# Optimization experiments

Measured on AMD Instinct MI355X. Metric: run time of the kernel, lower is better.

## Reference

```python
import jax, jax.numpy as jnp
import numpy as np

B, T1, T2 = 4, 768, 256
T = T1 + T2            # n_token
NI = T2                # n_i_token
D = 1024               # n_embd
H_MLP = 4096           # n_mlp_hidden
L = 12                 # n_layer
V = 512                # num_class / vocab_size
EPS = 1e-5


def _ln(x, g, b):
    m = jnp.mean(x, axis=-1, keepdims=True)
    v = jnp.mean((x - m) ** 2, axis=-1, keepdims=True)
    return (x - m) * jax.lax.rsqrt(v + EPS) * g + b


def setup_inputs() -> dict:
    key = jax.random.key(0)
    ks = jax.random.split(key, 16)
    s = 0.02
    return {
        "xt": jax.random.randint(ks[0], (B, T1), 0, V, dtype=jnp.int32),
        "zi": jax.random.randint(ks[1], (B, T2), 0, V, dtype=jnp.int32),
        "pos_emb": jax.random.normal(ks[2], (T, D), jnp.float32) * s,
        "t_emb": jax.random.normal(ks[3], (V, D), jnp.float32) * s,
        "i_emb": jax.random.normal(ks[4], (V, D), jnp.float32) * s,
        "ln1_g": jnp.ones((L, D), jnp.float32),
        "ln1_b": jnp.zeros((L, D), jnp.float32),
        "Wq": jax.random.normal(ks[5], (L, D, D), jnp.float32) * s,
        "Wk": jax.random.normal(ks[6], (L, D, D), jnp.float32) * s,
        "Wv": jax.random.normal(ks[7], (L, D, D), jnp.float32) * s,
        "ln2_g": jnp.ones((L, D), jnp.float32),
        "ln2_b": jnp.zeros((L, D), jnp.float32),
        "W1": jax.random.normal(ks[8], (L, D, H_MLP), jnp.float32) * s,
        "b1": jnp.zeros((L, H_MLP), jnp.float32),
        "W2": jax.random.normal(ks[9], (L, H_MLP, D), jnp.float32) * s,
        "b2": jnp.zeros((L, D), jnp.float32),
        "ro_W": jax.random.normal(ks[10], (D, V), jnp.float32) * s,
        "ro_b": jnp.zeros((V,), jnp.float32),
    }


def reference(xt, zi, pos_emb, t_emb, i_emb, ln1_g, ln1_b, Wq, Wk, Wv,
              ln2_g, ln2_b, W1, b1, W2, b2, ro_W, ro_b):
    # token + position embeddings: [B, T, D]
    H0 = jnp.concatenate([i_emb[zi], t_emb[xt]], axis=1) + pos_emb[None]
    scale = 1.0 / np.sqrt(D).astype(np.float32)

    def layer(H, p):
        g1, b1_, wq, wk, wv, g2, b2_, w1, bb1, w2, bb2 = p
        H1 = _ln(H, g1, b1_)
        q = H1 @ wq  # [B, T, D]
        k = H1 @ wk
        v = H1 @ wv
        attn = jax.nn.softmax(jnp.einsum('bid,bjd->bij', q, k) * scale, axis=-1)
        H = H + jnp.einsum('bij,bjd->bid', attn, v)
        # second application with extra rescale by embedding dim (H.shape[2] == D)
        H = H + jnp.einsum('bij,bjd->bid', attn / D, v)
        H2 = _ln(H, g2, b2_)
        H = H + jax.nn.gelu(H2 @ w1 + bb1, approximate=False) @ w2 + bb2
        return H, None

    params = (ln1_g, ln1_b, Wq, Wk, Wv, ln2_g, ln2_b, W1, b1, W2, b2)
    H, _ = jax.lax.scan(layer, H0, params)
    prediction = H @ ro_W + ro_b  # [B, T, V]
    return prediction[:, NI:, :]
```

## Files before the change

### kernel.cpp

```cpp
#include <hip/hip_runtime.h>
#include <hip/hip_bf16.h>
#include <math.h>

#define D_EMB  1024
#define T_TOK  1024
#define T1_TOK 768
#define T2_TOK 256
#define HMLP   4096
#define NLAYER 12
#define VCLS   512

typedef __attribute__((ext_vector_type(8))) short          short8;
typedef __attribute__((ext_vector_type(4))) float          f32x4;
typedef __attribute__((ext_vector_type(4))) unsigned short us4;
typedef unsigned short us;

__device__ __forceinline__ us f2bf(float f) {
    union { float f; unsigned int u; } c; c.f = f;
    unsigned int u = c.u;
    return (us)((u + 0x7FFFu + ((u >> 16) & 1u)) >> 16);
}

__device__ __forceinline__ void gld_lds16(const us* g, us* l) {
    __builtin_amdgcn_global_load_lds(
        (__attribute__((address_space(1))) void*)g,
        (__attribute__((address_space(3))) void*)l, 16, 0, 0);
}

__global__ __launch_bounds__(256)
void embed_kernel(const int* __restrict__ xt, const int* __restrict__ zi,
                  const float* __restrict__ pos, const float* __restrict__ temb,
                  const float* __restrict__ iemb, float* __restrict__ H)
{
    const long idx = (long)blockIdx.x * 256 + threadIdx.x;
    const long e   = idx * 4;
    const int  dd  = (int)(e & (D_EMB - 1));
    const long bt  = e >> 10;
    const int  t   = (int)(bt & (T_TOK - 1));
    const int  b   = (int)(bt >> 10);
    const float* src;
    if (t < T2_TOK) src = iemb + (long)zi[b * T2_TOK + t] * D_EMB + dd;
    else            src = temb + (long)xt[b * T1_TOK + (t - T2_TOK)] * D_EMB + dd;
    float4 sv = *(const float4*)src;
    float4 pv = *(const float4*)(pos + (long)t * D_EMB + dd);
    float4 o; o.x = sv.x + pv.x; o.y = sv.y + pv.y; o.z = sv.z + pv.z; o.w = sv.w + pv.w;
    *(float4*)(H + e) = o;
}

__global__ __launch_bounds__(256)
void ln_kernel(const float* __restrict__ X, const float* __restrict__ g,
               const float* __restrict__ b, us* __restrict__ Y)
{
    const long row = blockIdx.x;
    const int  tid = threadIdx.x;
    float4 v = *(const float4*)(X + row * D_EMB + tid * 4);
    float s = v.x + v.y + v.z + v.w;
    float q = v.x*v.x + v.y*v.y + v.z*v.z + v.w*v.w;
    #pragma unroll
    for (int o = 32; o >= 1; o >>= 1) { s += __shfl_down(s, o); q += __shfl_down(q, o); }
    __shared__ float rs[4], rq[4];
    const int w = tid >> 6;
    if ((tid & 63) == 0) { rs[w] = s; rq[w] = q; }
    __syncthreads();
    s = rs[0] + rs[1] + rs[2] + rs[3];
    q = rq[0] + rq[1] + rq[2] + rq[3];
    const float mean = s * (1.0f / D_EMB);
    const float var  = q * (1.0f / D_EMB) - mean * mean;
    const float rstd = rsqrtf(var + 1e-5f);
    float4 gg = *(const float4*)(g + tid * 4);
    float4 bb = *(const float4*)(b + tid * 4);
    us4 o;
    o.x = f2bf((v.x - mean) * rstd * gg.x + bb.x);
    o.y = f2bf((v.y - mean) * rstd * gg.y + bb.y);
    o.z = f2bf((v.z - mean) * rstd * gg.z + bb.z);
    o.w = f2bf((v.w - mean) * rstd * gg.w + bb.w);
    *(us4*)(Y + row * D_EMB + tid * 4) = o;
}

__global__ __launch_bounds__(256)
void softmax_kernel(const float* __restrict__ S, us* __restrict__ P)
{
    const long row = blockIdx.x;
    const int  tid = threadIdx.x;
    float4 v = *(const float4*)(S + row * T_TOK + tid * 4);
    const float sc = 0.03125f;
    float a = v.x * sc, b = v.y * sc, c = v.z * sc, d = v.w * sc;
    float mx = fmaxf(fmaxf(a, b), fmaxf(c, d));
    #pragma unroll
    for (int o = 32; o >= 1; o >>= 1) mx = fmaxf(mx, __shfl_down(mx, o));
    __shared__ float rm[4], rsum[4];
    const int w = tid >> 6;
    if ((tid & 63) == 0) rm[w] = mx;
    __syncthreads();
    mx = fmaxf(fmaxf(rm[0], rm[1]), fmaxf(rm[2], rm[3]));
    float e0 = expf(a - mx), e1 = expf(b - mx), e2 = expf(c - mx), e3 = expf(d - mx);
    float s = e0 + e1 + e2 + e3;
    #pragma unroll
    for (int o = 32; o >= 1; o >>= 1) s += __shfl_down(s, o);
    if ((tid & 63) == 0) rsum[w] = s;
    __syncthreads();
    s = rsum[0] + rsum[1] + rsum[2] + rsum[3];
    const float inv = 1.0f / s;
    us4 o4; o4.x = f2bf(e0 * inv); o4.y = f2bf(e1 * inv);
    o4.z = f2bf(e2 * inv); o4.w = f2bf(e3 * inv);
    *(us4*)(P + row * T_TOK + tid * 4) = o4;
}

__global__ __launch_bounds__(256)
void convT_kernel(const float* __restrict__ src, us* __restrict__ dst,
                  int K, int N)
{
    __shared__ us tile[32][33];
    const int tn = blockIdx.x, tk = blockIdx.y;
    const int tx = threadIdx.x & 31, ty = threadIdx.x >> 5;
    #pragma unroll
    for (int i = 0; i < 4; ++i) {
        const int r = ty + i * 8;
        tile[r][tx] = f2bf(src[(long)(tk * 32 + r) * N + tn * 32 + tx]);
    }
    __syncthreads();
    #pragma unroll
    for (int i = 0; i < 4; ++i) {
        const int r = ty + i * 8;
        dst[(long)(tn * 32 + r) * K + tk * 32 + tx] = tile[tx][r];
    }
}

__global__ __launch_bounds__(256)
void wconv_kernel(const float* __restrict__ Wq, const float* __restrict__ Wk,
                  const float* __restrict__ Wv, const float* __restrict__ W1,
                  const float* __restrict__ W2,
                  us* __restrict__ WqT, us* __restrict__ WkT,
                  us* __restrict__ WvT, us* __restrict__ W1T,
                  us* __restrict__ W2T)
{
    __shared__ us tile[64][66];
    const int t = blockIdx.x;
    const float* src; us* dst; int K, N, tk, tn;
    if (t < 768) {
        const int wsel = t >> 8, tt = t & 255;
        src = (wsel == 0) ? Wq : (wsel == 1) ? Wk : Wv;
        dst = (wsel == 0) ? WqT : (wsel == 1) ? WkT : WvT;
        K = 1024; N = 1024; tk = tt >> 4; tn = tt & 15;
    } else if (t < 1792) {
        const int tt = t - 768;
        src = W1; dst = W1T; K = 1024; N = 4096; tk = tt >> 6; tn = tt & 63;
    } else {
        const int tt = t - 1792;
        src = W2; dst = W2T; K = 4096; N = 1024; tk = tt >> 4; tn = tt & 15;
    }
    const int r  = threadIdx.x >> 4;
    const int c4 = threadIdx.x & 15;
    #pragma unroll
    for (int i = 0; i < 4; ++i) {
        const int row = r + i * 16;
        float4 v = *(const float4*)(src + (long)(tk * 64 + row) * N + tn * 64 + c4 * 4);
        tile[row][c4 * 4 + 0] = f2bf(v.x);
        tile[row][c4 * 4 + 1] = f2bf(v.y);
        tile[row][c4 * 4 + 2] = f2bf(v.z);
        tile[row][c4 * 4 + 3] = f2bf(v.w);
    }
    __syncthreads();
    #pragma unroll
    for (int i = 0; i < 4; ++i) {
        const int rr = r + i * 16;
        us4 o;
        o.x = tile[c4 * 4 + 0][rr];
        o.y = tile[c4 * 4 + 1][rr];
        o.z = tile[c4 * 4 + 2][rr];
        o.w = tile[c4 * 4 + 3][rr];
        *(us4*)(dst + (long)(tn * 64 + rr) * K + tk * 64 + c4 * 4) = o;
    }
}

__global__ __launch_bounds__(256)
void cvt_bf16_kernel(const float* __restrict__ X, us* __restrict__ Y)
{
    const long i = ((long)blockIdx.x * 256 + threadIdx.x) * 4;
    float4 v = *(const float4*)(X + i);
    us4 o; o.x = f2bf(v.x); o.y = f2bf(v.y); o.z = f2bf(v.z); o.w = f2bf(v.w);
    *(us4*)(Y + i) = o;
}

template<int EPI, int TN>
__global__ __launch_bounds__(512, 2)
void gemm8(const us* __restrict__ A, const us* __restrict__ B,
           void* __restrict__ C0, void* __restrict__ C1, void* __restrict__ C2,
           const float* __restrict__ bias,
           int N, int K, long sBz, float alpha)
{
    constexpr int FN   = TN / 32;
    constexpr int ABUF = 256 * 64;
    constexpr int BBUF = TN * 64;
    constexpr int BROW = (TN == 128) ? 16 : 8;
    __shared__ us As[3 * ABUF];
    __shared__ us Bs[3 * BBUF];

    const int gx = gridDim.x, gy = gridDim.y;
    const int o  = blockIdx.x + gx * blockIdx.y;
    const int nwg = gx * gy;
    const int virt = (nwg & 7) ? o : ((o & 7) * (nwg >> 3) + (o >> 3));
    const int ntile = virt / gy;
    const int mtile = virt - ntile * gy;
    const int m0 = mtile * 256, n0 = ntile * TN;

    const us* Bp = B + (long)(m0 >> 10) * sBz;

    const int tid  = threadIdx.x;
    const int lane = tid & 63, w = tid >> 6;
    const int srow = lane >> 3, sslot = (lane & 7) ^ srow;
    const int lr = lane & 15, hi = lane >> 4;
    const int wm = (w >> 1) * 64, wn = (w & 1) * (TN / 2);

    const us* gA = A + (long)(m0 + w * 32 + srow) * K + sslot * 8;
    const us* gB = Bp + (long)(n0 + w * BROW + srow) * K + sslot * 8;

    f32x4 acc[4][FN];
    #pragma unroll
    for (int f = 0; f < 4; ++f)
        #pragma unroll
        for (int g = 0; g < FN; ++g)
            acc[f][g] = (f32x4){0.f, 0.f, 0.f, 0.f};

    const int nk = K >> 6;

    #pragma unroll
    for (int tb = 0; tb < 2; ++tb) {
        #pragma unroll
        for (int j = 0; j < 4; ++j)
            gld_lds16(gA + (long)(j * 8) * K + tb * 64,
                      As + tb * ABUF + (w * 32 + j * 8) * 64);
        if constexpr (TN == 128) {
            #pragma unroll
            for (int j = 0; j < 2; ++j)
                gld_lds16(gB + (long)(j * 8) * K + tb * 64,
                          Bs + tb * BBUF + (w * 16 + j * 8) * 64);
        } else {
            gld_lds16(gB + tb * 64, Bs + tb * BBUF + (w * 8) * 64);
        }
    }
    if constexpr (TN == 128) asm volatile("s_waitcnt vmcnt(6)" ::: "memory");
    else                     asm volatile("s_waitcnt vmcnt(5)" ::: "memory");
    __builtin_amdgcn_s_barrier();

    for (int t = 0; t < nk; ++t) {
        const int cur = t % 3, nb = (t + 2) % 3;
        const us* Ac = As + cur * ABUF;
        const us* Bc = Bs + cur * BBUF;
        const int kk2 = (t + 2) << 6;
        #pragma unroll
        for (int kk = 0; kk < 2; ++kk) {
            short8 af[4], bg[FN];
            #pragma unroll
            for (int f = 0; f < 4; ++f) {
                const int rr = wm + f * 16 + lr;
                af[f] = *(const short8*)&Ac[rr * 64 + (((kk * 4 + hi) ^ (rr & 7)) * 8)];
            }
            #pragma unroll
            for (int g = 0; g < FN; ++g) {
                const int rn = wn + g * 16 + lr;
                bg[g] = *(const short8*)&Bc[rn * 64 + (((kk * 4 + hi) ^ (rn & 7)) * 8)];
            }
            if (t + 2 < nk) {
                gld_lds16(gA + (long)((kk * 2 + 0) * 8) * K + kk2,
                          As + nb * ABUF + (w * 32 + (kk * 2 + 0) * 8) * 64);
                gld_lds16(gA + (long)((kk * 2 + 1) * 8) * K + kk2,
                          As + nb * ABUF + (w * 32 + (kk * 2 + 1) * 8) * 64);
                if constexpr (TN == 128) {
                    gld_lds16(gB + (long)(kk * 8) * K + kk2,
                              Bs + nb * BBUF + (w * 16 + kk * 8) * 64);
                } else if (kk == 0) {
                    gld_lds16(gB + kk2, Bs + nb * BBUF + (w * 8) * 64);
                }
            }
            __builtin_amdgcn_s_barrier();
            asm volatile("s_waitcnt lgkmcnt(0)" ::: "memory");
            __builtin_amdgcn_sched_barrier(0);
            __builtin_amdgcn_s_setprio(1);
            #pragma unroll
            for (int f = 0; f < 4; ++f)
                #pragma unroll
                for (int g = 0; g < FN; ++g)
                    acc[f][g] = __builtin_amdgcn_mfma_f32_16x16x32_bf16(
                        af[f], bg[g], acc[f][g], 0, 0, 0);
            __builtin_amdgcn_s_setprio(0);
            __builtin_amdgcn_sched_barrier(0);
            if (kk == 1) {
                if (t + 2 < nk) {
                    if constexpr (TN == 128)
                        asm volatile("s_waitcnt vmcnt(6)" ::: "memory");
                    else
                        asm volatile("s_waitcnt vmcnt(5)" ::: "memory");
                } else if (t + 1 < nk) {
                    asm volatile("s_waitcnt vmcnt(0)" ::: "memory");
                }
            }
            __builtin_amdgcn_s_barrier();
        }
    }

    #pragma unroll
    for (int f = 0; f < 4; ++f) {
        #pragma unroll
        for (int g = 0; g < FN; ++g) {
            const int gm0 = m0 + wm + f * 16 + hi * 4;
            const int gn  = n0 + wn + g * 16 + lr;
            if constexpr (EPI == 7) {
                const int target = gn >> 10, col = gn & 1023;
                if (target == 2) {
                    us4 ov;
                    ov.x = f2bf(acc[f][g][0]); ov.y = f2bf(acc[f][g][1]);
                    ov.z = f2bf(acc[f][g][2]); ov.w = f2bf(acc[f][g][3]);
                    *(us4*)&((us*)C2)[(long)(gm0 >> 10) * (T_TOK * D_EMB)
                                      + (long)col * T_TOK + (gm0 & (T_TOK - 1))] = ov;
                } else {
                    us* dst = target ? (us*)C1 : (us*)C0;
                    #pragma unroll
                    for (int r = 0; r < 4; ++r)
                        dst[(long)(gm0 + r) * D_EMB + col] = f2bf(acc[f][g][r]);
                }
            } else if constexpr (EPI == 1) {
                #pragma unroll
                for (int r = 0; r < 4; ++r) {
                    float v = acc[f][g][r] + bias[gn];
                    const float ge = 0.5f * v * (1.0f + erff(v * 0.70710678118f));
                    ((us*)C0)[(long)(gm0 + r) * N + gn] = f2bf(ge);
                }
            } else if constexpr (EPI == 0) {
                #pragma unroll
                for (int r = 0; r < 4; ++r)
                    ((float*)C0)[(long)(gm0 + r) * N + gn] = acc[f][g][r];
            } else if constexpr (EPI == 2) {
                #pragma unroll
                for (int r = 0; r < 4; ++r) {
                    float* c = (float*)C0 + (long)(gm0 + r) * N + gn;
                    *c = *c + acc[f][g][r] + bias[gn];
                }
            } else {
                #pragma unroll
                for (int r = 0; r < 4; ++r) {
                    float* c = (float*)C0 + (long)(gm0 + r) * N + gn;
                    *c = *c + alpha * acc[f][g][r];
                }
            }
        }
    }
}

template<int EPI, int TN>
__global__ __launch_bounds__(256)
void gemm_bt(const us* __restrict__ A, const us* __restrict__ B0,
             void* __restrict__ C0, const float* __restrict__ bias,
             int M, int N, int K,
             long sAz, long sBz, long sCz, float alpha)
{
    constexpr int FN = TN / 32;
    constexpr int ABUF = 128 * 32;
    constexpr int BBUF = TN * 32;
    __shared__ us As[2 * ABUF];
    __shared__ us Bs[2 * BBUF];

    const us* Ap = A;
    const us* Bp = B0;

    const int gx = gridDim.x, gy = gridDim.y;
    const int o  = blockIdx.x + gx * blockIdx.y;
    const int nwg = gx * gy;
    const int virt = (nwg & 7) ? o : ((o & 7) * (nwg >> 3) + (o >> 3));
    const int ntile = virt / gy;
    int mtile = virt - ntile * gy;
    if constexpr (EPI == 4) mtile = (mtile / 6) * 8 + 2 + (mtile % 6);
    const int m0 = mtile * 128, n0 = ntile * TN;

    const int tid = threadIdx.x;
    const int l = tid & 63, w = tid >> 6;
    const int wm = (w >> 1) * 64, wn = (w & 1) * (TN / 2);
    const int lr = l & 15, hi = l >> 4;

    const int r0 = tid >> 2;
    const int s0 = (tid & 3) ^ ((r0 >> 1) & 3);
    const us* gA0 = Ap + (long)(m0 + r0) * K + s0 * 8;
    const us* gA1 = Ap + (long)(m0 + r0 + 64) * K + s0 * 8;
    const us* gB0 = Bp + (long)(n0 + r0) * K + s0 * 8;
    const int lA0 = w * 512, lA1 = 2048 + w * 512;
    const int lB0 = w * 512;

    f32x4 acc[4][FN];
    #pragma unroll
    for (int f = 0; f < 4; ++f)
        #pragma unroll
        for (int gq = 0; gq < FN; ++gq)
            acc[f][gq] = (f32x4){0.f, 0.f, 0.f, 0.f};

    const int nk = K >> 5;
    gld_lds16(gA0, As + lA0);
    gld_lds16(gA1, As + lA1);
    gld_lds16(gB0, Bs + lB0);
    __syncthreads();

    for (int t = 0; t < nk; ++t) {
        const int cur = t & 1;
        const int aB = (cur ^ 1) * ABUF, bB = (cur ^ 1) * BBUF;
        if (t + 1 < nk) {
            const int k1 = (t + 1) << 5;
            gld_lds16(gA0 + k1, As + aB + lA0);
            gld_lds16(gA1 + k1, As + aB + lA1);
            gld_lds16(gB0 + k1, Bs + bB + lB0);
        }
        const int aC = cur * ABUF, bC = cur * BBUF;
        short8 af[4], bg[FN];
        #pragma unroll
        for (int f = 0; f < 4; ++f) {
            const int rr = wm + f * 16 + lr;
            const int sl = hi ^ ((rr >> 1) & 3);
            af[f] = *(const short8*)&As[aC + rr * 32 + sl * 8];
        }
        #pragma unroll
        for (int gq = 0; gq < FN; ++gq) {
            const int rn = wn + gq * 16 + lr;
            const int sl = hi ^ ((rn >> 1) & 3);
            bg[gq] = *(const short8*)&Bs[bC + rn * 32 + sl * 8];
        }
        #pragma unroll
        for (int f = 0; f < 4; ++f)
            #pragma unroll
            for (int gq = 0; gq < FN; ++gq)
                acc[f][gq] = __builtin_amdgcn_mfma_f32_16x16x32_bf16(
                    af[f], bg[gq], acc[f][gq], 0, 0, 0);
        __syncthreads();
    }

    #pragma unroll
    for (int f = 0; f < 4; ++f) {
        #pragma unroll
        for (int gq = 0; gq < FN; ++gq) {
            #pragma unroll
            for (int r = 0; r < 4; ++r) {
                const int gm = m0 + wm + f * 16 + hi * 4 + r;
                const int gn = n0 + wn + gq * 16 + lr;
                const int tt = gm & (T_TOK - 1);
                ((float*)C0)[(long)((gm >> 10) * T1_TOK + (tt - T2_TOK)) * VCLS + gn]
                    = acc[f][gq][r] + bias[gn];
            }
        }
    }
}

extern "C" void kernel_launch(void* const* d_in, const int* in_sizes, int n_in,
                              void* d_out, int out_size, void* d_ws, size_t ws_size,
                              hipStream_t stream)
{
    (void)in_sizes; (void)n_in; (void)out_size; (void)ws_size;
    const int*   xt   = (const int*)d_in[0];
    const int*   zi   = (const int*)d_in[1];
    const float* pos  = (const float*)d_in[2];
    const float* temb = (const float*)d_in[3];
    const float* iemb = (const float*)d_in[4];
    const float* ln1g = (const float*)d_in[5];
    const float* ln1b = (const float*)d_in[6];
    const float* Wq   = (const float*)d_in[7];
    const float* Wk   = (const float*)d_in[8];
    const float* Wv   = (const float*)d_in[9];
    const float* ln2g = (const float*)d_in[10];
    const float* ln2b = (const float*)d_in[11];
    const float* W1   = (const float*)d_in[12];
    const float* b1   = (const float*)d_in[13];
    const float* W2   = (const float*)d_in[14];
    const float* b2   = (const float*)d_in[15];
    const float* roW  = (const float*)d_in[16];
    const float* rob  = (const float*)d_in[17];
    float* out = (float*)d_out;

    char* wsb = (char*)d_ws;
    float* H    = (float*)(wsb + 0);
    us*    LNb  = (us*)(wsb + 16777216);
    float* S    = (float*)(wsb + 25165824);
    us*    Qb   = (us*)(wsb + 41943040);
    us*    Kb   = (us*)(wsb + 50331648);
    us*    VT   = (us*)(wsb + 58720256);
    us*    Pb   = (us*)(wsb + 67108864);
    us*    Hid  = (us*)(wsb + 41943040);
    us*    WqT  = (us*)(wsb + 75497472);
    us*    WkT  = (us*)(wsb + 77594624);
    us*    WvT  = (us*)(wsb + 79691776);
    us*    W1T  = (us*)(wsb + 81788928);
    us*    W2T  = (us*)(wsb + 90177536);
    us*    roWT = W1T;
    us*    Hbf  = LNb;

    const long TD = (long)T_TOK * D_EMB;

    embed_kernel<<<4096, 256, 0, stream>>>(xt, zi, pos, temb, iemb, H);

    for (int lyr = 0; lyr < NLAYER; ++lyr) {
        const long dd = (long)lyr * D_EMB * D_EMB;
        const long d1 = (long)lyr * D_EMB * HMLP;
        wconv_kernel<<<2816, 256, 0, stream>>>(
            Wq + dd, Wk + dd, Wv + dd, W1 + d1, W2 + d1,
            WqT, WkT, WvT, W1T, W2T);
        ln_kernel<<<4096, 256, 0, stream>>>(H, ln1g + lyr * D_EMB, ln1b + lyr * D_EMB, LNb);
        gemm8<7, 64><<<dim3(48, 16, 1), 512, 0, stream>>>(
            LNb, WqT, Qb, Kb, VT, nullptr, 3072, D_EMB, 0L, 1.f);
        gemm8<0, 64><<<dim3(16, 16, 1), 512, 0, stream>>>(
            Qb, Kb, S, nullptr, nullptr, nullptr, T_TOK, D_EMB, TD, 1.f);
        softmax_kernel<<<4096, 256, 0, stream>>>(S, Pb);
        gemm8<3, 64><<<dim3(16, 16, 1), 512, 0, stream>>>(
            Pb, VT, H, nullptr, nullptr, nullptr, D_EMB, T_TOK, TD,
            1.0f + 1.0f / (float)D_EMB);
        ln_kernel<<<4096, 256, 0, stream>>>(H, ln2g + lyr * D_EMB, ln2b + lyr * D_EMB, LNb);
        gemm8<1, 128><<<dim3(32, 16, 1), 512, 0, stream>>>(
            LNb, W1T, Hid, nullptr, nullptr, b1 + (long)lyr * HMLP,
            HMLP, D_EMB, 0L, 1.f);
        gemm8<2, 64><<<dim3(16, 16, 1), 512, 0, stream>>>(
            Hid, W2T, H, nullptr, nullptr, b2 + (long)lyr * D_EMB,
            D_EMB, HMLP, 0L, 1.f);
    }
    cvt_bf16_kernel<<<4096, 256, 0, stream>>>(H, Hbf);
    convT_kernel<<<dim3(16, 32), 256, 0, stream>>>(roW, roWT, D_EMB, VCLS);
    gemm_bt<4, 64><<<dim3(8, 24, 1), 256, 0, stream>>>(
        Hbf, roWT, out, rob, 4096, VCLS, D_EMB, 0L, 0L, 0L, 1.f);
}
```

Before: 3.051 ms.

## Convert all layer weights in one upfront launch and remap GEMM tile order

Replaces the twelve per-layer weight transpose/bf16 conversion launches with one 2D-grid launch that converts every layer's weights into separate workspace regions before the layer loop. The read-out weight conversion also moves ahead of the loop, since it no longer shares the W1T buffer. The GEMM tile index mapping changes from column-major to row-major over the grid, which alters which tiles run concurrently and so changes L2 reuse. The cost is a much larger workspace holding bf16 copies of all layers' weights, about 300MB.

```diff
diff --git a/kernel.cpp b/kernel.cpp
--- a/kernel.cpp
+++ b/kernel.cpp
@@ -127,27 +127,31 @@
 }
 
 __global__ __launch_bounds__(256)
-void wconv_kernel(const float* __restrict__ Wq, const float* __restrict__ Wk,
-                  const float* __restrict__ Wv, const float* __restrict__ W1,
-                  const float* __restrict__ W2,
-                  us* __restrict__ WqT, us* __restrict__ WkT,
-                  us* __restrict__ WvT, us* __restrict__ W1T,
-                  us* __restrict__ W2T)
+void wconv_all_kernel(const float* __restrict__ Wq, const float* __restrict__ Wk,
+                      const float* __restrict__ Wv, const float* __restrict__ W1,
+                      const float* __restrict__ W2,
+                      us* __restrict__ WqkvT, us* __restrict__ W1T,
+                      us* __restrict__ W2T)
 {
     __shared__ us tile[64][66];
+    const int lyr = blockIdx.y;
     const int t = blockIdx.x;
     const float* src; us* dst; int K, N, tk, tn;
     if (t < 768) {
         const int wsel = t >> 8, tt = t & 255;
-        src = (wsel == 0) ? Wq : (wsel == 1) ? Wk : Wv;
-        dst = (wsel == 0) ? WqT : (wsel == 1) ? WkT : WvT;
+        src = ((wsel == 0) ? Wq : (wsel == 1) ? Wk : Wv) + (long)lyr * D_EMB * D_EMB;
+        dst = WqkvT + (long)lyr * 3072 * 1024 + (long)wsel * (1024 * 1024);
         K = 1024; N = 1024; tk = tt >> 4; tn = tt & 15;
     } else if (t < 1792) {
         const int tt = t - 768;
-        src = W1; dst = W1T; K = 1024; N = 4096; tk = tt >> 6; tn = tt & 63;
+        src = W1 + (long)lyr * D_EMB * HMLP;
+        dst = W1T + (long)lyr * (long)HMLP * D_EMB;
+        K = 1024; N = 4096; tk = tt >> 6; tn = tt & 63;
     } else {
         const int tt = t - 1792;
-        src = W2; dst = W2T; K = 4096; N = 1024; tk = tt >> 4; tn = tt & 15;
+        src = W2 + (long)lyr * D_EMB * HMLP;
+        dst = W2T + (long)lyr * (long)D_EMB * HMLP;
+        K = 4096; N = 1024; tk = tt >> 4; tn = tt & 15;
     }
     const int r  = threadIdx.x >> 4;
     const int c4 = threadIdx.x & 15;
@@ -200,8 +204,8 @@
     const int o  = blockIdx.x + gx * blockIdx.y;
     const int nwg = gx * gy;
     const int virt = (nwg & 7) ? o : ((o & 7) * (nwg >> 3) + (o >> 3));
-    const int ntile = virt / gy;
-    const int mtile = virt - ntile * gy;
+    const int mtile = virt / gx;
+    const int ntile = virt - mtile * gx;
     const int m0 = mtile * 256, n0 = ntile * TN;
 
     const us* Bp = B + (long)(m0 >> 10) * sBz;
@@ -480,27 +484,26 @@
     us*    VT   = (us*)(wsb + 58720256);
     us*    Pb   = (us*)(wsb + 67108864);
     us*    Hid  = (us*)(wsb + 41943040);
-    us*    WqT  = (us*)(wsb + 75497472);
-    us*    WkT  = (us*)(wsb + 77594624);
-    us*    WvT  = (us*)(wsb + 79691776);
-    us*    W1T  = (us*)(wsb + 81788928);
-    us*    W2T  = (us*)(wsb + 90177536);
-    us*    roWT = W1T;
+    us*    roWT = (us*)(wsb + 75497472);
+    us*    WqkvT= (us*)(wsb + 83886080);
+    us*    W1T  = (us*)(wsb + 159383552);
+    us*    W2T  = (us*)(wsb + 260046848);
     us*    Hbf  = LNb;
 
     const long TD = (long)T_TOK * D_EMB;
 
+    wconv_all_kernel<<<dim3(2816, 12), 256, 0, stream>>>(
+        Wq, Wk, Wv, W1, W2, WqkvT, W1T, W2T);
+    convT_kernel<<<dim3(16, 32), 256, 0, stream>>>(roW, roWT, D_EMB, VCLS);
     embed_kernel<<<4096, 256, 0, stream>>>(xt, zi, pos, temb, iemb, H);
 
     for (int lyr = 0; lyr < NLAYER; ++lyr) {
-        const long dd = (long)lyr * D_EMB * D_EMB;
-        const long d1 = (long)lyr * D_EMB * HMLP;
-        wconv_kernel<<<2816, 256, 0, stream>>>(
-            Wq + dd, Wk + dd, Wv + dd, W1 + d1, W2 + d1,
-            WqT, WkT, WvT, W1T, W2T);
+        const us* Wqkv_l = WqkvT + (long)lyr * 3072 * 1024;
+        const us* W1_l   = W1T + (long)lyr * (long)HMLP * D_EMB;
+        const us* W2_l   = W2T + (long)lyr * (long)D_EMB * HMLP;
         ln_kernel<<<4096, 256, 0, stream>>>(H, ln1g + lyr * D_EMB, ln1b + lyr * D_EMB, LNb);
         gemm8<7, 64><<<dim3(48, 16, 1), 512, 0, stream>>>(
-            LNb, WqT, Qb, Kb, VT, nullptr, 3072, D_EMB, 0L, 1.f);
+            LNb, Wqkv_l, Qb, Kb, VT, nullptr, 3072, D_EMB, 0L, 1.f);
         gemm8<0, 64><<<dim3(16, 16, 1), 512, 0, stream>>>(
             Qb, Kb, S, nullptr, nullptr, nullptr, T_TOK, D_EMB, TD, 1.f);
         softmax_kernel<<<4096, 256, 0, stream>>>(S, Pb);
@@ -509,14 +512,13 @@
             1.0f + 1.0f / (float)D_EMB);
         ln_kernel<<<4096, 256, 0, stream>>>(H, ln2g + lyr * D_EMB, ln2b + lyr * D_EMB, LNb);
         gemm8<1, 128><<<dim3(32, 16, 1), 512, 0, stream>>>(
-            LNb, W1T, Hid, nullptr, nullptr, b1 + (long)lyr * HMLP,
+            LNb, W1_l, Hid, nullptr, nullptr, b1 + (long)lyr * HMLP,
             HMLP, D_EMB, 0L, 1.f);
         gemm8<2, 64><<<dim3(16, 16, 1), 512, 0, stream>>>(
-            Hid, W2T, H, nullptr, nullptr, b2 + (long)lyr * D_EMB,
+            Hid, W2_l, H, nullptr, nullptr, b2 + (long)lyr * D_EMB,
             D_EMB, HMLP, 0L, 1.f);
     }
     cvt_bf16_kernel<<<4096, 256, 0, stream>>>(H, Hbf);
-    convT_kernel<<<dim3(16, 32), 256, 0, stream>>>(roW, roWT, D_EMB, VCLS);
     gemm_bt<4, 64><<<dim3(8, 24, 1), 256, 0, stream>>>(
         Hbf, roWT, out, rob, 4096, VCLS, D_EMB, 0L, 0L, 0L, 1.f);
 }
```

New measurement: 3.268 ms. 1.07x slower.

## Add 256x256-tile GEMM for MLP layers with split-K atomics for W2

Applied to the files above, without the earlier changes.

Adds a new gemm256 kernel using 256x256 output tiles, a 4-stage LDS pipeline with explicit waitcnt/barrier scheduling, and MFMA 16x16x32. The W1 GEMM (with GELU epilogue) and the W2 GEMM now use it; W2 is split along K into 4 slices accumulated into H with float atomics, bias added only by the first slice. The larger tiles raise data reuse per block, and split-K keeps enough blocks in flight for the narrow-N W2 GEMM. The cost is atomic traffic, a summation order that is no longer fixed, and higher register pressure. The Q/K/V weight buffers are also merged into one pointer, which is a cleanup.

```diff
diff --git a/kernel.cpp b/kernel.cpp
--- a/kernel.cpp
+++ b/kernel.cpp
@@ -130,8 +130,7 @@
 void wconv_kernel(const float* __restrict__ Wq, const float* __restrict__ Wk,
                   const float* __restrict__ Wv, const float* __restrict__ W1,
                   const float* __restrict__ W2,
-                  us* __restrict__ WqT, us* __restrict__ WkT,
-                  us* __restrict__ WvT, us* __restrict__ W1T,
+                  us* __restrict__ WqkvT, us* __restrict__ W1T,
                   us* __restrict__ W2T)
 {
     __shared__ us tile[64][66];
@@ -140,7 +139,7 @@
     if (t < 768) {
         const int wsel = t >> 8, tt = t & 255;
         src = (wsel == 0) ? Wq : (wsel == 1) ? Wk : Wv;
-        dst = (wsel == 0) ? WqT : (wsel == 1) ? WkT : WvT;
+        dst = WqkvT + (long)wsel * (1024 * 1024);
         K = 1024; N = 1024; tk = tt >> 4; tn = tt & 15;
     } else if (t < 1792) {
         const int tt = t - 768;
@@ -180,6 +179,122 @@
     float4 v = *(const float4*)(X + i);
     us4 o; o.x = f2bf(v.x); o.y = f2bf(v.y); o.z = f2bf(v.z); o.w = f2bf(v.w);
     *(us4*)(Y + i) = o;
+}
+
+template<int EPI>
+__global__ __launch_bounds__(512, 2)
+void gemm256(const us* __restrict__ A, const us* __restrict__ B,
+             void* __restrict__ C, const float* __restrict__ bias,
+             int N, int K, int kLen)
+{
+    constexpr int HBUF = 256 * 32;
+    __shared__ us As[4 * HBUF];
+    __shared__ us Bs[4 * HBUF];
+
+    const int z = blockIdx.z;
+    const int kOff = z * kLen;
+
+    const int gx = gridDim.x, gy = gridDim.y;
+    const int o  = blockIdx.x + gx * blockIdx.y;
+    const int nwg = gx * gy;
+    const int virt = (o & 7) * (nwg >> 3) + (o >> 3);
+    const int ntile = virt / gy;
+    const int mtile = virt - ntile * gy;
+    const int m0 = mtile * 256, n0 = ntile * 256;
+
+    const int tid  = threadIdx.x;
+    const int lane = tid & 63, w = tid >> 6;
+    const int lr = lane & 15, hi = lane >> 4;
+    const int wm = (w >> 2) * 128, wn = (w & 3) * 64;
+
+    const int srow0 = tid >> 2;
+    const int sslot = tid & 3;
+    const int swz0  = sslot ^ ((srow0 >> 1) & 3);
+    const int srow1 = srow0 + 128;
+    const int swz1  = sslot ^ ((srow1 >> 1) & 3);
+    const us* gA0 = A + (long)(m0 + srow0) * K + kOff + swz0 * 8;
+    const us* gA1 = A + (long)(m0 + srow1) * K + kOff + swz1 * 8;
+    const us* gB0 = B + (long)(n0 + srow0) * K + kOff + swz0 * 8;
+    const us* gB1 = B + (long)(n0 + srow1) * K + kOff + swz1 * 8;
+    const int lds0 = (w * 64) * 8;
+    const int lds1 = (512 + w * 64) * 8;
+
+    f32x4 acc[8][4];
+    #pragma unroll
+    for (int f = 0; f < 8; ++f)
+        #pragma unroll
+        for (int g = 0; g < 4; ++g)
+            acc[f][g] = (f32x4){0.f, 0.f, 0.f, 0.f};
+
+    const int nh = kLen >> 5;
+    auto STAGE = [&](int h) {
+        const int s = h & 3;
+        const long kb = (long)h << 5;
+        gld_lds16(gA0 + kb, As + s * HBUF + lds0);
+        gld_lds16(gA1 + kb, As + s * HBUF + lds1);
+        gld_lds16(gB0 + kb, Bs + s * HBUF + lds0);
+        gld_lds16(gB1 + kb, Bs + s * HBUF + lds1);
+    };
+
+    STAGE(0); STAGE(1); STAGE(2);
+    asm volatile("s_waitcnt vmcnt(8)" ::: "memory");
+    __builtin_amdgcn_s_barrier();
+
+    for (int h = 0; h < nh; ++h) {
+        const int s = h & 3;
+        const us* Ac = As + s * HBUF;
+        const us* Bc = Bs + s * HBUF;
+        short8 af[8], bg[4];
+        #pragma unroll
+        for (int f = 0; f < 8; ++f) {
+            const int rr = wm + f * 16 + lr;
+            af[f] = *(const short8*)&Ac[rr * 32 + ((hi ^ ((rr >> 1) & 3)) * 8)];
+        }
+        #pragma unroll
+        for (int g = 0; g < 4; ++g) {
+            const int rn = wn + g * 16 + lr;
+            bg[g] = *(const short8*)&Bc[rn * 32 + ((hi ^ ((rn >> 1) & 3)) * 8)];
+        }
+        if (h + 3 < nh) STAGE(h + 3);
+        __builtin_amdgcn_s_barrier();
+        asm volatile("s_waitcnt lgkmcnt(0)" ::: "memory");
+        __builtin_amdgcn_sched_barrier(0);
+        __builtin_amdgcn_s_setprio(1);
+        #pragma unroll
+        for (int f = 0; f < 8; ++f)
+            #pragma unroll
+            for (int g = 0; g < 4; ++g)
+                acc[f][g] = __builtin_amdgcn_mfma_f32_16x16x32_bf16(
+                    af[f], bg[g], acc[f][g], 0, 0, 0);
+        __builtin_amdgcn_s_setprio(0);
+        __builtin_amdgcn_sched_barrier(0);
+        if (h + 3 < nh)      asm volatile("s_waitcnt vmcnt(8)" ::: "memory");
+        else if (h + 2 < nh) asm volatile("s_waitcnt vmcnt(4)" ::: "memory");
+        else if (h + 1 < nh) asm volatile("s_waitcnt vmcnt(0)" ::: "memory");
+        __builtin_amdgcn_s_barrier();
+    }
+
+    #pragma unroll
+    for (int f = 0; f < 8; ++f) {
+        #pragma unroll
+        for (int g = 0; g < 4; ++g) {
+            const int gm0 = m0 + wm + f * 16 + hi * 4;
+            const int gn  = n0 + wn + g * 16 + lr;
+            if constexpr (EPI == 1) {
+                #pragma unroll
+                for (int r = 0; r < 4; ++r) {
+                    float v = acc[f][g][r] + bias[gn];
+                    const float ge = 0.5f * v * (1.0f + erff(v * 0.70710678118f));
+                    ((us*)C)[(long)(gm0 + r) * N + gn] = f2bf(ge);
+                }
+            } else {
+                #pragma unroll
+                for (int r = 0; r < 4; ++r)
+                    atomicAdd((float*)C + (long)(gm0 + r) * N + gn,
+                              acc[f][g][r] + ((z == 0) ? bias[gn] : 0.f));
+            }
+        }
+    }
 }
 
 template<int EPI, int TN>
@@ -319,23 +434,10 @@
                     for (int r = 0; r < 4; ++r)
                         dst[(long)(gm0 + r) * D_EMB + col] = f2bf(acc[f][g][r]);
                 }
-            } else if constexpr (EPI == 1) {
-                #pragma unroll
-                for (int r = 0; r < 4; ++r) {
-                    float v = acc[f][g][r] + bias[gn];
-                    const float ge = 0.5f * v * (1.0f + erff(v * 0.70710678118f));
-                    ((us*)C0)[(long)(gm0 + r) * N + gn] = f2bf(ge);
-                }
             } else if constexpr (EPI == 0) {
                 #pragma unroll
                 for (int r = 0; r < 4; ++r)
                     ((float*)C0)[(long)(gm0 + r) * N + gn] = acc[f][g][r];
-            } else if constexpr (EPI == 2) {
-                #pragma unroll
-                for (int r = 0; r < 4; ++r) {
-                    float* c = (float*)C0 + (long)(gm0 + r) * N + gn;
-                    *c = *c + acc[f][g][r] + bias[gn];
-                }
             } else {
                 #pragma unroll
                 for (int r = 0; r < 4; ++r) {
@@ -359,9 +461,6 @@
     constexpr int BBUF = TN * 32;
     __shared__ us As[2 * ABUF];
     __shared__ us Bs[2 * BBUF];
-
-    const us* Ap = A;
-    const us* Bp = B0;
 
     const int gx = gridDim.x, gy = gridDim.y;
     const int o  = blockIdx.x + gx * blockIdx.y;
@@ -379,9 +478,9 @@
 
     const int r0 = tid >> 2;
     const int s0 = (tid & 3) ^ ((r0 >> 1) & 3);
-    const us* gA0 = Ap + (long)(m0 + r0) * K + s0 * 8;
-    const us* gA1 = Ap + (long)(m0 + r0 + 64) * K + s0 * 8;
-    const us* gB0 = Bp + (long)(n0 + r0) * K + s0 * 8;
+    const us* gA0 = A + (long)(m0 + r0) * K + s0 * 8;
+    const us* gA1 = A + (long)(m0 + r0 + 64) * K + s0 * 8;
+    const us* gB0 = B0 + (long)(n0 + r0) * K + s0 * 8;
     const int lA0 = w * 512, lA1 = 2048 + w * 512;
     const int lB0 = w * 512;
 
@@ -480,9 +579,7 @@
     us*    VT   = (us*)(wsb + 58720256);
     us*    Pb   = (us*)(wsb + 67108864);
     us*    Hid  = (us*)(wsb + 41943040);
-    us*    WqT  = (us*)(wsb + 75497472);
-    us*    WkT  = (us*)(wsb + 77594624);
-    us*    WvT  = (us*)(wsb + 79691776);
+    us*    WqkvT= (us*)(wsb + 75497472);
     us*    W1T  = (us*)(wsb + 81788928);
     us*    W2T  = (us*)(wsb + 90177536);
     us*    roWT = W1T;
@@ -496,11 +593,10 @@
         const long dd = (long)lyr * D_EMB * D_EMB;
         const long d1 = (long)lyr * D_EMB * HMLP;
         wconv_kernel<<<2816, 256, 0, stream>>>(
-            Wq + dd, Wk + dd, Wv + dd, W1 + d1, W2 + d1,
-            WqT, WkT, WvT, W1T, W2T);
+            Wq + dd, Wk + dd, Wv + dd, W1 + d1, W2 + d1, WqkvT, W1T, W2T);
         ln_kernel<<<4096, 256, 0, stream>>>(H, ln1g + lyr * D_EMB, ln1b + lyr * D_EMB, LNb);
         gemm8<7, 64><<<dim3(48, 16, 1), 512, 0, stream>>>(
-            LNb, WqT, Qb, Kb, VT, nullptr, 3072, D_EMB, 0L, 1.f);
+            LNb, WqkvT, Qb, Kb, VT, nullptr, 3072, D_EMB, 0L, 1.f);
         gemm8<0, 64><<<dim3(16, 16, 1), 512, 0, stream>>>(
             Qb, Kb, S, nullptr, nullptr, nullptr, T_TOK, D_EMB, TD, 1.f);
         softmax_kernel<<<4096, 256, 0, stream>>>(S, Pb);
@@ -508,12 +604,10 @@
             Pb, VT, H, nullptr, nullptr, nullptr, D_EMB, T_TOK, TD,
             1.0f + 1.0f / (float)D_EMB);
         ln_kernel<<<4096, 256, 0, stream>>>(H, ln2g + lyr * D_EMB, ln2b + lyr * D_EMB, LNb);
-        gemm8<1, 128><<<dim3(32, 16, 1), 512, 0, stream>>>(
-            LNb, W1T, Hid, nullptr, nullptr, b1 + (long)lyr * HMLP,
-            HMLP, D_EMB, 0L, 1.f);
-        gemm8<2, 64><<<dim3(16, 16, 1), 512, 0, stream>>>(
-            Hid, W2T, H, nullptr, nullptr, b2 + (long)lyr * D_EMB,
-            D_EMB, HMLP, 0L, 1.f);
+        gemm256<1><<<dim3(16, 16, 1), 512, 0, stream>>>(
+            LNb, W1T, Hid, b1 + (long)lyr * HMLP, HMLP, D_EMB, D_EMB);
+        gemm256<6><<<dim3(4, 16, 4), 512, 0, stream>>>(
+            Hid, W2T, H, b2 + (long)lyr * D_EMB, D_EMB, HMLP, HMLP / 4);
     }
     cvt_bf16_kernel<<<4096, 256, 0, stream>>>(H, Hbf);
     convT_kernel<<<dim3(16, 32), 256, 0, stream>>>(roW, roWT, D_EMB, VCLS);
```

New measurement: 3.372 ms. +10.5%, slower.
